# Kernel tuning notes

Measured on AMD Instinct MI355X. Metric: run time of the kernel, lower is better.

Reference implementation:

```python
import jax, jax.numpy as jnp
import numpy as np

N = 20000
E = 320000
F_IN = 50
HID = 64          # hidden_channels
HEADS = 8
WIDTH = HID * HEADS  # 512
NUM_CLASSES = 121


def setup_inputs() -> dict:
    key = jax.random.key(0)
    ks = jax.random.split(key, 16)
    def p(k, shape, fan_in):
        return (jax.random.normal(k, shape, dtype=jnp.float32) / np.sqrt(fan_in)).astype(jnp.float32)
    x = jax.random.normal(ks[0], (N, F_IN), dtype=jnp.float32)
    edge_index = jax.random.randint(ks[1], (2, E), 0, N, dtype=jnp.int64)
    return {
        "x": x,
        "edge_index": edge_index,
        # layer 1: 50 -> 64, heads=8, concat
        "W1": p(ks[2], (F_IN, HEADS * HID), F_IN),
        "a1_src": p(ks[3], (HEADS, HID), HID),
        "a1_dst": p(ks[4], (HEADS, HID), HID),
        "b1": jnp.zeros((HEADS * HID,), jnp.float32),
        # layer 2: 512 -> 512, heads=1, concat
        "W2": p(ks[5], (WIDTH, WIDTH), WIDTH),
        "a2_src": p(ks[6], (1, WIDTH), WIDTH),
        "a2_dst": p(ks[7], (1, WIDTH), WIDTH),
        "b2": jnp.zeros((WIDTH,), jnp.float32),
        # layer 3: 512 -> 121, heads=1, concat=False (mean)
        "W3": p(ks[8], (WIDTH, NUM_CLASSES), WIDTH),
        "a3_src": p(ks[9], (1, NUM_CLASSES), NUM_CLASSES),
        "a3_dst": p(ks[10], (1, NUM_CLASSES), NUM_CLASSES),
        "b3": jnp.zeros((NUM_CLASSES,), jnp.float32),
    }


def gat_conv(x, src, dst, W, a_src, a_dst, b, heads, out_ch, concat):
    n = x.shape[0]
    h = (x @ W).reshape(n, heads, out_ch)                 # [N, H, C]
    al_s = jnp.sum(h * a_src, axis=-1)                     # [N, H]
    al_d = jnp.sum(h * a_dst, axis=-1)                     # [N, H]
    e = jax.nn.leaky_relu(al_s[src] + al_d[dst], 0.2)      # [E, H]
    # edge softmax per destination node (stable)
    m = jax.ops.segment_max(e, dst, num_segments=n)        # [N, H]
    m = jnp.where(jnp.isfinite(m), m, 0.0)
    ex = jnp.exp(e - m[dst])
    z = jax.ops.segment_sum(ex, dst, num_segments=n)       # [N, H]
    alpha = ex / (z[dst] + 1e-16)                          # [E, H]
    msg = h[src] * alpha[..., None]                        # [E, H, C]
    out = jax.ops.segment_sum(msg, dst, num_segments=n)    # [N, H, C]
    out = out.reshape(n, heads * out_ch) if concat else out.mean(axis=1)
    return out + b


def reference(x, edge_index, W1, a1_src, a1_dst, b1, W2, a2_src, a2_dst, b2, W3, a3_src, a3_dst, b3):
    n = x.shape[0]
    # PyG GATConv adds self loops by default
    loops = jnp.arange(n, dtype=edge_index.dtype)
    src = jnp.concatenate([edge_index[0], loops])
    dst = jnp.concatenate([edge_index[1], loops])
    # eval mode: dropout is identity
    x1 = gat_conv(x, src, dst, W1, a1_src, a1_dst, b1, HEADS, HID, True)
    h = jax.nn.elu(x1)
    x1 = gat_conv(h, src, dst, W2, a2_src, a2_dst, b2, 1, WIDTH, True)
    h = jax.nn.elu(x1)
    x1 = gat_conv(h, src, dst, W3, a3_src, a3_dst, b3, 1, NUM_CLASSES, False)
    return x1
```

## Files before the change

kernel.cpp:

```cpp
#include <hip/hip_runtime.h>
#include <hip/hip_bf16.h>
#include <hip/hip_fp16.h>

#define NN     20000
#define ERAW   320000
#define ETOT   (ERAW + NN)
#define F_IN   50
#define HID    64
#define HEADS  8
#define WIDTH  512
#define NCLS   121
#define NCLS_P 128

typedef __attribute__((ext_vector_type(8))) __bf16 bf16x8;
typedef __attribute__((ext_vector_type(4))) float floatx4;

__device__ __forceinline__ unsigned short f32_to_bf16_rn(float f) {
  unsigned u = __float_as_uint(f);
  unsigned r = u + 0x7fffu + ((u >> 16) & 1u);
  return (unsigned short)(r >> 16);
}
__device__ __forceinline__ void split_one(float f, unsigned short& h,
                                          unsigned short& l) {
  h = f32_to_bf16_rn(f);
  float fh = __uint_as_float(((unsigned)h) << 16);
  l = f32_to_bf16_rn(f - fh);
}

__device__ __forceinline__ float2 u2f2(unsigned u) {
  __half2 hv = *reinterpret_cast<__half2*>(&u);
  return __half22float2(hv);
}

__device__ __forceinline__ void gll16(const unsigned short* g,
                                      const unsigned short* l) {
  __builtin_amdgcn_global_load_lds(
      (const __attribute__((address_space(1))) unsigned int*)(const void*)g,
      (__attribute__((address_space(3))) unsigned int*)(void*)l, 16, 0, 0);
}

#define PW_BLOCKS 449
__global__ __launch_bounds__(256) void prep_weights(
    const float* __restrict__ W1, const float* __restrict__ W2,
    const float* __restrict__ W3, const float* __restrict__ a1s,
    const float* __restrict__ a1d, unsigned short* __restrict__ w1hHi,
    unsigned short* __restrict__ w1hLo, unsigned short* __restrict__ w2tHi,
    unsigned short* __restrict__ w2tLo, unsigned short* __restrict__ w3tHi,
    unsigned short* __restrict__ w3tLo, float* __restrict__ w1as,
    float* __restrict__ w1ad) {
  __shared__ float t[32][33];
  const int b = blockIdx.x;
  if (b < 320) {
    const float* W;
    unsigned short *thi, *tlo;
    int M, Mp, bx, by;
    const int K = WIDTH;
    if (b < 256) {
      W = W2; thi = w2tHi; tlo = w2tLo; M = WIDTH; Mp = WIDTH;
      bx = b & 15; by = b >> 4;
    } else {
      int bb = b - 256;
      W = W3; thi = w3tHi; tlo = w3tLo; M = NCLS; Mp = NCLS_P;
      bx = bb & 15; by = bb >> 4;
    }
    int k0 = bx * 32, m0 = by * 32;
    int tx = threadIdx.x & 31, ty = threadIdx.x >> 5;
    #pragma unroll
    for (int r = 0; r < 4; ++r) {
      int k = k0 + ty + r * 8, m = m0 + tx;
      float v = 0.f;
      if (k < K && m < M) v = W[(size_t)k * M + m];
      t[ty + r * 8][tx] = v;
    }
    __syncthreads();
    #pragma unroll
    for (int r = 0; r < 4; ++r) {
      int m = m0 + ty + r * 8, k = k0 + tx;
      if (m < Mp && k < K) {
        unsigned short h, l;
        split_one(t[tx][ty + r * 8], h, l);
        thi[(size_t)m * K + k] = h;
        tlo[(size_t)m * K + k] = l;
      }
    }
  } else if (b < 448) {
    int idx = (b - 320) * 256 + threadIdx.x;
    if (idx < HEADS * HID * HID) {
      int hd = idx >> 12, rem = idx & 4095;
      int col = rem >> 6, k = rem & 63;
      float v = (k < F_IN) ? W1[(size_t)k * WIDTH + hd * HID + col] : 0.f;
      unsigned short h, l;
      split_one(v, h, l);
      w1hHi[idx] = h;
      w1hLo[idx] = l;
    }
  } else {
    for (int idx = threadIdx.x; idx < 2 * F_IN * HEADS; idx += 256) {
      int which = idx >= F_IN * HEADS;
      int r = which ? idx - F_IN * HEADS : idx;
      int k = r >> 3, h = r & 7;
      const float* a = which ? a1d : a1s;
      float s = 0.f;
      for (int c = 0; c < HID; ++c)
        s += W1[(size_t)k * WIDTH + h * HID + c] * a[h * HID + c];
      (which ? w1ad : w1as)[r] = s;
    }
  }
}

__global__ __launch_bounds__(256) void gemm_split_db(
    const unsigned short* __restrict__ Ahi, const unsigned short* __restrict__ Alo,
    const unsigned short* __restrict__ Bthi, const unsigned short* __restrict__ Btlo,
    __half* __restrict__ C16, int N, int K, int M, int Mp, int RB, int CB) {
  __shared__ unsigned short lds[32768];

  const int f = blockIdx.x;
  const int xcd = f & 7;
  const int g = f >> 3;
  const int cb = g % CB;
  const int rb = (g / CB) * 8 + xcd;
  if (rb >= RB) return;
  const int r0 = rb * 128, c0 = cb * 128;

  const int tid = threadIdx.x;
  const int wave = tid >> 6, lane = tid & 63;
  const int wr = wave >> 1, wc = wave & 1;
  const int lkg = lane >> 4, lmn = lane & 15;

  const int rquad = lane >> 2, slot = lane & 3;
  const unsigned short* abase =
      (wave == 0) ? Ahi : (wave == 1) ? Alo : (wave == 2) ? Bthi : Btlo;
  const bool isA = wave < 2;
  const unsigned short* gsrc[8];
  int ldsoff[8];
  #pragma unroll
  for (int i = 0; i < 8; ++i) {
    int r = i * 16 + rquad;
    int c = slot ^ ((r >> 1) & 3);
    size_t grow;
    if (isA) {
      int ra = r0 + r;
      if (ra > N - 1) ra = N - 1;
      grow = (size_t)ra;
    } else {
      grow = (size_t)(c0 + r);
    }
    gsrc[i] = abase + grow * K + c * 8;
    ldsoff[i] = wave * 4096 + i * 512;
  }

  int offA[4], offB[4];
  #pragma unroll
  for (int mi = 0; mi < 4; ++mi) {
    int m = wr * 64 + mi * 16 + lmn;
    offA[mi] = m * 32 + (lkg ^ ((m >> 1) & 3)) * 8;
  }
  #pragma unroll
  for (int ni = 0; ni < 4; ++ni) {
    int n = wc * 64 + ni * 16 + lmn;
    offB[ni] = 8192 + n * 32 + (lkg ^ ((n >> 1) & 3)) * 8;
  }

  floatx4 acc[4][4] = {};

  #pragma unroll
  for (int i = 0; i < 8; ++i) gll16(gsrc[i], lds + ldsoff[i]);

  const int nk = K >> 5;
  for (int t = 0; t < nk; ++t) {
    if (t + 1 < nk) {
      const unsigned short* dst = lds + ((t + 1) & 1) * 16384;
      #pragma unroll
      for (int i = 0; i < 8; ++i)
        gll16(gsrc[i] + (t + 1) * 32, dst + ldsoff[i]);
      asm volatile("s_waitcnt vmcnt(8)" ::: "memory");
    } else {
      asm volatile("s_waitcnt vmcnt(0)" ::: "memory");
    }
    __builtin_amdgcn_sched_barrier(0);
    __builtin_amdgcn_s_barrier();
    __builtin_amdgcn_sched_barrier(0);

    const unsigned short* Lb = lds + (t & 1) * 16384;
    bf16x8 fAhi[4], fAlo[4], fBhi[4], fBlo[4];
    #pragma unroll
    for (int mi = 0; mi < 4; ++mi) {
      fAhi[mi] = *(const bf16x8*)(Lb + offA[mi]);
      fAlo[mi] = *(const bf16x8*)(Lb + 4096 + offA[mi]);
    }
    #pragma unroll
    for (int ni = 0; ni < 4; ++ni) {
      fBhi[ni] = *(const bf16x8*)(Lb + offB[ni]);
      fBlo[ni] = *(const bf16x8*)(Lb + 4096 + offB[ni]);
    }
    #pragma unroll
    for (int mi = 0; mi < 4; ++mi)
      #pragma unroll
      for (int ni = 0; ni < 4; ++ni) {
        acc[mi][ni] = __builtin_amdgcn_mfma_f32_16x16x32_bf16(
            fAhi[mi], fBhi[ni], acc[mi][ni], 0, 0, 0);
        acc[mi][ni] = __builtin_amdgcn_mfma_f32_16x16x32_bf16(
            fAhi[mi], fBlo[ni], acc[mi][ni], 0, 0, 0);
        acc[mi][ni] = __builtin_amdgcn_mfma_f32_16x16x32_bf16(
            fAlo[mi], fBhi[ni], acc[mi][ni], 0, 0, 0);
      }

    __builtin_amdgcn_sched_barrier(0);
    asm volatile("s_waitcnt lgkmcnt(0)" ::: "memory");
    __builtin_amdgcn_s_barrier();
    __builtin_amdgcn_sched_barrier(0);
  }

  #pragma unroll
  for (int mi = 0; mi < 4; ++mi) {
    #pragma unroll
    for (int r = 0; r < 4; ++r) {
      int grow = r0 + wr * 64 + mi * 16 + (lane >> 4) * 4 + r;
      if (grow >= N) continue;
      #pragma unroll
      for (int ni = 0; ni < 4; ++ni) {
        int gcol = c0 + wc * 64 + ni * 16 + lmn;
        float v = (gcol < M) ? acc[mi][ni][r] : 0.f;
        C16[(size_t)grow * Mp + gcol] = __float2half(v);
      }
    }
  }
}

__global__ __launch_bounds__(256) void gemm_l1_heads(
    const unsigned short* __restrict__ Ahi, const unsigned short* __restrict__ Alo,
    const unsigned short* __restrict__ Bthi, const unsigned short* __restrict__ Btlo,
    unsigned short* __restrict__ outHi, unsigned short* __restrict__ outLo,
    const float* __restrict__ bias) {
  __shared__ unsigned short sAhi[8192], sAlo[8192], sBhi[4096], sBlo[4096];
  const int tid = threadIdx.x;
  const int wave = tid >> 6, lane = tid & 63;
  const int r0 = blockIdx.x * 128;
  const int hd = blockIdx.y;
  const int lkg = lane >> 4, lmn = lane & 15;

  #pragma unroll
  for (int t = 0; t < 4; ++t) {
    int cid = tid + t * 256;
    int row = cid >> 3, c = cid & 7;
    int gr = r0 + row; if (gr > NN - 1) gr = NN - 1;
    const size_t goff = (size_t)gr * WIDTH + hd * HID + c * 8;
    int loff = (((c >> 2) * 4 + (c & 3)) * 128 + row) * 8;
    *(uint4*)(sAhi + loff) = *(const uint4*)(Ahi + goff);
    *(uint4*)(sAlo + loff) = *(const uint4*)(Alo + goff);
  }
  #pragma unroll
  for (int t = 0; t < 2; ++t) {
    int cid = tid + t * 256;
    int col = cid >> 3, c = cid & 7;
    const size_t goff = (size_t)(hd * HID + col) * HID + c * 8;
    int loff = (((c >> 2) * 4 + (c & 3)) * 64 + col) * 8;
    *(uint4*)(sBhi + loff) = *(const uint4*)(Bthi + goff);
    *(uint4*)(sBlo + loff) = *(const uint4*)(Btlo + goff);
  }
  __syncthreads();

  floatx4 acc[2][4] = {};
  #pragma unroll
  for (int ks = 0; ks < 2; ++ks) {
    bf16x8 fAhi[2], fAlo[2], fBhi[4], fBlo[4];
    #pragma unroll
    for (int mi = 0; mi < 2; ++mi) {
      int m = wave * 32 + mi * 16 + lmn;
      int off = ((ks * 4 + lkg) * 128 + m) * 8;
      fAhi[mi] = *(const bf16x8*)(sAhi + off);
      fAlo[mi] = *(const bf16x8*)(sAlo + off);
    }
    #pragma unroll
    for (int ni = 0; ni < 4; ++ni) {
      int n = ni * 16 + lmn;
      int off = ((ks * 4 + lkg) * 64 + n) * 8;
      fBhi[ni] = *(const bf16x8*)(sBhi + off);
      fBlo[ni] = *(const bf16x8*)(sBlo + off);
    }
    #pragma unroll
    for (int mi = 0; mi < 2; ++mi)
      #pragma unroll
      for (int ni = 0; ni < 4; ++ni) {
        acc[mi][ni] = __builtin_amdgcn_mfma_f32_16x16x32_bf16(
            fAhi[mi], fBhi[ni], acc[mi][ni], 0, 0, 0);
        acc[mi][ni] = __builtin_amdgcn_mfma_f32_16x16x32_bf16(
            fAhi[mi], fBlo[ni], acc[mi][ni], 0, 0, 0);
        acc[mi][ni] = __builtin_amdgcn_mfma_f32_16x16x32_bf16(
            fAlo[mi], fBhi[ni], acc[mi][ni], 0, 0, 0);
      }
  }

  #pragma unroll
  for (int mi = 0; mi < 2; ++mi) {
    #pragma unroll
    for (int r = 0; r < 4; ++r) {
      int grow = r0 + wave * 32 + mi * 16 + (lane >> 4) * 4 + r;
      if (grow >= NN) continue;
      #pragma unroll
      for (int ni = 0; ni < 4; ++ni) {
        int gcol = hd * HID + ni * 16 + lmn;
        float v = acc[mi][ni][r] + bias[gcol];
        v = (v > 0.f) ? v : (__expf(v) - 1.0f);
        unsigned short hh, ll;
        split_one(v, hh, ll);
        outHi[(size_t)grow * WIDTH + gcol] = hh;
        outLo[(size_t)grow * WIDTH + gcol] = ll;
      }
    }
  }
}

__global__ __launch_bounds__(256) void al1_kernel(
    const float* __restrict__ x, const float* __restrict__ w1as,
    const float* __restrict__ w1ad, float* __restrict__ al_s,
    float* __restrict__ al_d) {
  int n = (blockIdx.x * blockDim.x + threadIdx.x) >> 6;
  int lane = threadIdx.x & 63;
  if (n >= NN) return;
  float xv = (lane < F_IN) ? x[(size_t)n * F_IN + lane] : 0.f;
  float ws[HEADS], wd[HEADS];
  #pragma unroll
  for (int h = 0; h < HEADS; ++h) {
    ws[h] = (lane < F_IN) ? w1as[lane * HEADS + h] : 0.f;
    wd[h] = (lane < F_IN) ? w1ad[lane * HEADS + h] : 0.f;
  }
  #pragma unroll
  for (int h = 0; h < HEADS; ++h) {
    float ss = xv * ws[h], sd = xv * wd[h];
    #pragma unroll
    for (int o = 32; o; o >>= 1) {
      ss += __shfl_xor(ss, o);
      sd += __shfl_xor(sd, o);
    }
    if (lane == 0) {
      al_s[n * HEADS + h] = ss;
      al_d[n * HEADS + h] = sd;
    }
  }
}

template <int C, int CS>
__global__ __launch_bounds__(256) void compute_al16(
    const __half* __restrict__ h16, const float* __restrict__ a_src,
    const float* __restrict__ a_dst, float* __restrict__ al_s,
    float* __restrict__ al_d) {
  int n = (blockIdx.x * blockDim.x + threadIdx.x) >> 6;
  int lane = threadIdx.x & 63;
  if (n >= NN) return;
  const __half* hr = h16 + (size_t)n * CS;
  float ss = 0.f, sd = 0.f;
  if (C % 512 == 0) {
    uint4 raw = *(const uint4*)(hr + lane * 8);
    float f[8];
    float2 t;
    t = u2f2(raw.x); f[0] = t.x; f[1] = t.y;
    t = u2f2(raw.y); f[2] = t.x; f[3] = t.y;
    t = u2f2(raw.z); f[4] = t.x; f[5] = t.y;
    t = u2f2(raw.w); f[6] = t.x; f[7] = t.y;
    #pragma unroll
    for (int j = 0; j < 8; ++j) {
      int c = lane * 8 + j;
      ss += f[j] * a_src[c];
      sd += f[j] * a_dst[c];
    }
  } else {
    for (int c = lane; c < C; c += 64) {
      float v = __half2float(hr[c]);
      ss += v * a_src[c];
      sd += v * a_dst[c];
    }
  }
  #pragma unroll
  for (int o = 32; o; o >>= 1) {
    ss += __shfl_xor(ss, o);
    sd += __shfl_xor(sd, o);
  }
  if (lane == 0) {
    al_s[n] = ss;
    al_d[n] = sd;
  }
}

__global__ __launch_bounds__(256) void count_deg(
    const int* __restrict__ edst, int* __restrict__ deg) {
  int e = blockIdx.x * blockDim.x + threadIdx.x;
  if (e >= ETOT) return;
  int d = (e < ERAW) ? edst[e] : (e - ERAW);
  atomicAdd(&deg[d], 1);
}

__global__ __launch_bounds__(256) void scan_deg(
    const int* __restrict__ deg, int* __restrict__ rowptr) {
  __shared__ int part[256];
  const int t = threadIdx.x;
  const int CHUNK = (NN + 255) / 256;
  int lo = t * CHUNK, hi = min(lo + CHUNK, NN);
  int s = 0;
  for (int i = lo; i < hi; ++i) s += deg[i];
  part[t] = s;
  __syncthreads();
  for (int off = 1; off < 256; off <<= 1) {
    int v = (t >= off) ? part[t - off] : 0;
    __syncthreads();
    part[t] += v;
    __syncthreads();
  }
  int base = (t == 0) ? 0 : part[t - 1];
  for (int i = lo; i < hi; ++i) {
    rowptr[i] = base;
    base += deg[i];
  }
  if (t == 255) rowptr[NN] = part[255];
}

__global__ __launch_bounds__(256) void scatter_csr(
    const int* __restrict__ esrc, const int* __restrict__ edst,
    const int* __restrict__ rowptr, int* __restrict__ cnt,
    int* __restrict__ csrc) {
  int e = blockIdx.x * blockDim.x + threadIdx.x;
  if (e >= ETOT) return;
  int s, d;
  if (e < ERAW) { s = esrc[e]; d = edst[e]; }
  else          { s = e - ERAW; d = e - ERAW; }
  int pos = rowptr[d] + atomicAdd(&cnt[d], 1);
  csrc[pos] = s;
}

__global__ __launch_bounds__(256) void agg_x_sm(
    const int* __restrict__ rowptr, const int* __restrict__ csrc,
    const float* __restrict__ al_s, const float* __restrict__ al_d,
    const float* __restrict__ x, unsigned short* __restrict__ outHi,
    unsigned short* __restrict__ outLo) {
  const int w = threadIdx.x >> 6, lane = threadIdx.x & 63;
  const int d = blockIdx.x * 4 + w;
  if (d >= NN) return;
  const int r0 = rowptr[d], r1 = rowptr[d + 1];
  const int mh = lane & 7;
  const float ald_my = al_d[d * HEADS + mh];
  float m_my = al_s[d * HEADS + mh] + ald_my;
  m_my = (m_my > 0.f) ? m_my : 0.2f * m_my;

  float z_my = 0.f;
  float acc[HEADS];
  #pragma unroll
  for (int hh = 0; hh < HEADS; ++hh) acc[hh] = 0.f;
  for (int p = r0; p < r1; ++p) {
    int s = csrc[p];
    float v = al_s[s * HEADS + mh] + ald_my;
    v = (v > 0.f) ? v : 0.2f * v;
    float a = __expf(v - m_my);
    z_my += a;
    float xv = (lane < F_IN) ? x[(size_t)s * F_IN + lane] : 0.f;
    #pragma unroll
    for (int hh = 0; hh < HEADS; ++hh) acc[hh] += __shfl(a, hh, 8) * xv;
  }
  #pragma unroll
  for (int hh = 0; hh < HEADS; ++hh) {
    float zh = __shfl(z_my, hh, 8);
    float v = (lane < F_IN) ? acc[hh] / (zh + 1e-16f) : 0.f;
    unsigned short h2, l2;
    split_one(v, h2, l2);
    outHi[(size_t)d * WIDTH + hh * HID + lane] = h2;
    outLo[(size_t)d * WIDTH + hh * HID + lane] = l2;
  }
}

template <int M, int MS, bool ELU, bool SPLIT>
__global__ __launch_bounds__(256) void pull_agg_sm(
    const int* __restrict__ rowptr, const int* __restrict__ csrc,
    const float* __restrict__ al_s, const float* __restrict__ al_d,
    const __half* __restrict__ h16, const float* __restrict__ bias,
    float* __restrict__ out, unsigned short* __restrict__ outHi,
    unsigned short* __restrict__ outLo) {
  constexpr int EPL = MS / 64;
  const int w = threadIdx.x >> 6;
  const int lane = threadIdx.x & 63;
  const int d = blockIdx.x * 4 + w;
  if (d >= NN) return;
  const int r0 = rowptr[d], r1 = rowptr[d + 1];
  const float ald = al_d[d];
  float m = al_s[d] + ald;
  m = (m > 0.f) ? m : 0.2f * m;

  const int base = lane * EPL;
  const __half* hb = h16 + base;
  float acc[EPL];
  #pragma unroll
  for (int j = 0; j < EPL; ++j) acc[j] = 0.f;
  float z = 0.f;

  int p = r0;
  for (; p + 8 <= r1; p += 8) {
    int s[8];
    #pragma unroll
    for (int j = 0; j < 8; ++j) s[j] = csrc[p + j];
    uint4 raw8[8];
    unsigned raw2[8];
    #pragma unroll
    for (int j = 0; j < 8; ++j) {
      const __half* hr = hb + (size_t)s[j] * MS;
      if (EPL == 8)      raw8[j] = *(const uint4*)hr;
      else if (EPL == 2) raw2[j] = *(const unsigned*)hr;
    }
    float av[8];
    #pragma unroll
    for (int j = 0; j < 8; ++j) av[j] = al_s[s[j]];
    #pragma unroll
    for (int j = 0; j < 8; ++j) {
      float v = av[j] + ald;
      v = (v > 0.f) ? v : 0.2f * v;
      float a = __expf(v - m);
      z += a;
      if (EPL == 8) {
        float2 f0 = u2f2(raw8[j].x), f1 = u2f2(raw8[j].y);
        float2 f2 = u2f2(raw8[j].z), f3 = u2f2(raw8[j].w);
        acc[0] += f0.x * a; acc[1] += f0.y * a;
        acc[2] += f1.x * a; acc[3] += f1.y * a;
        acc[4] += f2.x * a; acc[5] += f2.y * a;
        acc[6] += f3.x * a; acc[7] += f3.y * a;
      } else if (EPL == 2) {
        float2 f0 = u2f2(raw2[j]);
        acc[0] += f0.x * a;
        acc[1] += f0.y * a;
      }
    }
  }
  for (; p < r1; ++p) {
    int s = csrc[p];
    float v = al_s[s] + ald;
    v = (v > 0.f) ? v : 0.2f * v;
    float a = __expf(v - m);
    z += a;
    const __half* hr = hb + (size_t)s * MS;
    if (EPL == 8) {
      uint4 raw = *(const uint4*)hr;
      float2 f0 = u2f2(raw.x), f1 = u2f2(raw.y);
      float2 f2 = u2f2(raw.z), f3 = u2f2(raw.w);
      acc[0] += f0.x * a; acc[1] += f0.y * a;
      acc[2] += f1.x * a; acc[3] += f1.y * a;
      acc[4] += f2.x * a; acc[5] += f2.y * a;
      acc[6] += f3.x * a; acc[7] += f3.y * a;
    } else if (EPL == 2) {
      unsigned raw = *(const unsigned*)hr;
      float2 f0 = u2f2(raw);
      acc[0] += f0.x * a;
      acc[1] += f0.y * a;
    }
  }
  const float iz = 1.0f / (z + 1e-16f);

  #pragma unroll
  for (int j = 0; j < EPL; ++j) {
    if ((M == MS) || (base + j < M)) {
      float v = acc[j] * iz + bias[base + j];
      if (ELU) v = (v > 0.f) ? v : (__expf(v) - 1.0f);
      if (SPLIT) {
        unsigned short hh, ll;
        split_one(v, hh, ll);
        outHi[(size_t)d * M + base + j] = hh;
        outLo[(size_t)d * M + base + j] = ll;
      } else {
        out[(size_t)d * M + base + j] = v;
      }
    }
  }
}

extern "C" void kernel_launch(void* const* d_in, const int* in_sizes, int n_in,
                              void* d_out, int out_size, void* d_ws,
                              size_t ws_size, hipStream_t stream) {
  const float* x      = (const float*)d_in[0];
  const int*   ei     = (const int*)d_in[1];
  const float* W1     = (const float*)d_in[2];
  const float* a1_src = (const float*)d_in[3];
  const float* a1_dst = (const float*)d_in[4];
  const float* b1     = (const float*)d_in[5];
  const float* W2     = (const float*)d_in[6];
  const float* a2_src = (const float*)d_in[7];
  const float* a2_dst = (const float*)d_in[8];
  const float* b2     = (const float*)d_in[9];
  const float* W3     = (const float*)d_in[10];
  const float* a3_src = (const float*)d_in[11];
  const float* a3_dst = (const float*)d_in[12];
  const float* b3     = (const float*)d_in[13];
  float* out = (float*)d_out;

  const int* esrc = ei;
  const int* edst = ei + ERAW;

  unsigned short* p1Hi  = (unsigned short*)d_ws;
  unsigned short* p1Lo  = p1Hi + (size_t)NN * WIDTH;
  unsigned short* p2Hi  = p1Lo + (size_t)NN * WIDTH;
  unsigned short* p2Lo  = p2Hi + (size_t)NN * WIDTH;
  __half*        h16    = (__half*)(p2Lo + (size_t)NN * WIDTH);
  unsigned short* w1hHi = (unsigned short*)(h16 + (size_t)NN * WIDTH);
  unsigned short* w1hLo = w1hHi + (size_t)HEADS * HID * HID;
  unsigned short* w2tHi = w1hLo + (size_t)HEADS * HID * HID;
  unsigned short* w2tLo = w2tHi + (size_t)WIDTH * WIDTH;
  unsigned short* w3tHi = w2tLo + (size_t)WIDTH * WIDTH;
  unsigned short* w3tLo = w3tHi + (size_t)NCLS_P * WIDTH;
  float* al_s   = (float*)(w3tLo + (size_t)NCLS_P * WIDTH);
  float* al_d   = al_s + (size_t)NN * HEADS;
  float* w1as   = al_d + (size_t)NN * HEADS;
  float* w1ad   = w1as + F_IN * HEADS;
  int* deg      = (int*)(w1ad + F_IN * HEADS);
  int* cnt      = deg + NN;
  int* rowptr   = cnt + NN;
  int* csrc     = rowptr + NN + 4;

  hipMemsetAsync(deg, 0, (size_t)(2 * NN) * sizeof(int), stream);
  const int eblk = (ETOT + 255) / 256;
  count_deg<<<eblk, 256, 0, stream>>>(edst, deg);
  scan_deg<<<1, 256, 0, stream>>>(deg, rowptr);
  scatter_csr<<<eblk, 256, 0, stream>>>(esrc, edst, rowptr, cnt, csrc);

  prep_weights<<<PW_BLOCKS, 256, 0, stream>>>(
      W1, W2, W3, a1_src, a1_dst, w1hHi, w1hLo, w2tHi, w2tLo, w3tHi, w3tLo,
      w1as, w1ad);

  const int nwblk = (NN + 3) / 4;

  al1_kernel<<<nwblk, 256, 0, stream>>>(x, w1as, w1ad, al_s, al_d);
  agg_x_sm<<<nwblk, 256, 0, stream>>>(rowptr, csrc, al_s, al_d, x, p1Hi,
                                      p1Lo);
  gemm_l1_heads<<<dim3((NN + 127) / 128, HEADS), 256, 0, stream>>>(
      p1Hi, p1Lo, w1hHi, w1hLo, p2Hi, p2Lo, b1);

  const int RB = (NN + 127) / 128;
  const int RBG = (RB + 7) / 8;

  gemm_split_db<<<RBG * 8 * (WIDTH / 128), 256, 0, stream>>>(
      p2Hi, p2Lo, w2tHi, w2tLo, h16, NN, WIDTH, WIDTH, WIDTH, RB, WIDTH / 128);
  compute_al16<WIDTH, WIDTH><<<nwblk, 256, 0, stream>>>(h16, a2_src, a2_dst,
                                                        al_s, al_d);
  pull_agg_sm<WIDTH, WIDTH, true, true><<<nwblk, 256, 0, stream>>>(
      rowptr, csrc, al_s, al_d, h16, b2, nullptr, p1Hi, p1Lo);

  gemm_split_db<<<RBG * 8 * (NCLS_P / 128), 256, 0, stream>>>(
      p1Hi, p1Lo, w3tHi, w3tLo, h16, NN, WIDTH, NCLS, NCLS_P, RB,
      NCLS_P / 128);
  compute_al16<NCLS, NCLS_P><<<nwblk, 256, 0, stream>>>(h16, a3_src, a3_dst,
                                                        al_s, al_d);
  pull_agg_sm<NCLS, NCLS_P, false, false><<<nwblk, 256, 0, stream>>>(
      rowptr, csrc, al_s, al_d, h16, b3, out, nullptr, nullptr);
}
```

Measured before the change: 398.9 us.

## Double GEMM K-tile to 64 with 8-way swizzle and batch edge loads in agg_x

The split-bf16 GEMM now stages a K-slice of 64 instead of 32 per iteration. It doubles LDS to 128 KB, switches to an 8-slot XOR swizzle, and runs two MFMA sub-steps per barrier pair, so barrier and wait overhead per unit of work is halved. The layer-1 aggregation kernel unrolls the edge loop by 8 and issues all neighbour index, feature and attention loads before computing, to expose more memory-level parallelism. The larger LDS footprint cuts blocks per CU and may hurt occupancy and latency hiding.

```diff
diff --git a/kernel.cpp b/kernel.cpp
--- a/kernel.cpp
+++ b/kernel.cpp
@@ -112,7 +112,7 @@
     const unsigned short* __restrict__ Ahi, const unsigned short* __restrict__ Alo,
     const unsigned short* __restrict__ Bthi, const unsigned short* __restrict__ Btlo,
     __half* __restrict__ C16, int N, int K, int M, int Mp, int RB, int CB) {
-  __shared__ unsigned short lds[32768];
+  __shared__ unsigned short lds[65536];
 
   const int f = blockIdx.x;
   const int xcd = f & 7;
@@ -127,16 +127,16 @@
   const int wr = wave >> 1, wc = wave & 1;
   const int lkg = lane >> 4, lmn = lane & 15;
 
-  const int rquad = lane >> 2, slot = lane & 3;
+  const int row8 = lane >> 3, cslot = lane & 7;
   const unsigned short* abase =
       (wave == 0) ? Ahi : (wave == 1) ? Alo : (wave == 2) ? Bthi : Btlo;
   const bool isA = wave < 2;
-  const unsigned short* gsrc[8];
-  int ldsoff[8];
-  #pragma unroll
-  for (int i = 0; i < 8; ++i) {
-    int r = i * 16 + rquad;
-    int c = slot ^ ((r >> 1) & 3);
+  const unsigned short* gsrc[16];
+  int ldsoff[16];
+  #pragma unroll
+  for (int i = 0; i < 16; ++i) {
+    int r = i * 8 + row8;
+    int c = cslot ^ (r & 7);
     size_t grow;
     if (isA) {
       int ra = r0 + r;
@@ -146,34 +146,34 @@
       grow = (size_t)(c0 + r);
     }
     gsrc[i] = abase + grow * K + c * 8;
-    ldsoff[i] = wave * 4096 + i * 512;
-  }
-
-  int offA[4], offB[4];
+    ldsoff[i] = wave * 8192 + i * 512;
+  }
+
+  int rowA[4], m7A[4], rowB[4], m7B[4];
   #pragma unroll
   for (int mi = 0; mi < 4; ++mi) {
     int m = wr * 64 + mi * 16 + lmn;
-    offA[mi] = m * 32 + (lkg ^ ((m >> 1) & 3)) * 8;
+    rowA[mi] = m * 64;  m7A[mi] = m & 7;
   }
   #pragma unroll
   for (int ni = 0; ni < 4; ++ni) {
     int n = wc * 64 + ni * 16 + lmn;
-    offB[ni] = 8192 + n * 32 + (lkg ^ ((n >> 1) & 3)) * 8;
+    rowB[ni] = 16384 + n * 64;  m7B[ni] = n & 7;
   }
 
   floatx4 acc[4][4] = {};
 
   #pragma unroll
-  for (int i = 0; i < 8; ++i) gll16(gsrc[i], lds + ldsoff[i]);
-
-  const int nk = K >> 5;
+  for (int i = 0; i < 16; ++i) gll16(gsrc[i], lds + ldsoff[i]);
+
+  const int nk = K >> 6;
   for (int t = 0; t < nk; ++t) {
     if (t + 1 < nk) {
-      const unsigned short* dst = lds + ((t + 1) & 1) * 16384;
-      #pragma unroll
-      for (int i = 0; i < 8; ++i)
-        gll16(gsrc[i] + (t + 1) * 32, dst + ldsoff[i]);
-      asm volatile("s_waitcnt vmcnt(8)" ::: "memory");
+      const unsigned short* dst = lds + ((t + 1) & 1) * 32768;
+      #pragma unroll
+      for (int i = 0; i < 16; ++i)
+        gll16(gsrc[i] + (t + 1) * 64, dst + ldsoff[i]);
+      asm volatile("s_waitcnt vmcnt(16)" ::: "memory");
     } else {
       asm volatile("s_waitcnt vmcnt(0)" ::: "memory");
     }
@@ -181,29 +181,34 @@
     __builtin_amdgcn_s_barrier();
     __builtin_amdgcn_sched_barrier(0);
 
-    const unsigned short* Lb = lds + (t & 1) * 16384;
-    bf16x8 fAhi[4], fAlo[4], fBhi[4], fBlo[4];
-    #pragma unroll
-    for (int mi = 0; mi < 4; ++mi) {
-      fAhi[mi] = *(const bf16x8*)(Lb + offA[mi]);
-      fAlo[mi] = *(const bf16x8*)(Lb + 4096 + offA[mi]);
-    }
-    #pragma unroll
-    for (int ni = 0; ni < 4; ++ni) {
-      fBhi[ni] = *(const bf16x8*)(Lb + offB[ni]);
-      fBlo[ni] = *(const bf16x8*)(Lb + 4096 + offB[ni]);
-    }
-    #pragma unroll
-    for (int mi = 0; mi < 4; ++mi)
+    const unsigned short* Lb = lds + (t & 1) * 32768;
+    #pragma unroll
+    for (int ksub = 0; ksub < 2; ++ksub) {
+      bf16x8 fAhi[4], fAlo[4], fBhi[4], fBlo[4];
+      #pragma unroll
+      for (int mi = 0; mi < 4; ++mi) {
+        int s = rowA[mi] + (((ksub << 2) | lkg) ^ m7A[mi]) * 8;
+        fAhi[mi] = *(const bf16x8*)(Lb + s);
+        fAlo[mi] = *(const bf16x8*)(Lb + s + 8192);
+      }
       #pragma unroll
       for (int ni = 0; ni < 4; ++ni) {
-        acc[mi][ni] = __builtin_amdgcn_mfma_f32_16x16x32_bf16(
-            fAhi[mi], fBhi[ni], acc[mi][ni], 0, 0, 0);
-        acc[mi][ni] = __builtin_amdgcn_mfma_f32_16x16x32_bf16(
-            fAhi[mi], fBlo[ni], acc[mi][ni], 0, 0, 0);
-        acc[mi][ni] = __builtin_amdgcn_mfma_f32_16x16x32_bf16(
-            fAlo[mi], fBhi[ni], acc[mi][ni], 0, 0, 0);
-      }
+        int s = rowB[ni] + (((ksub << 2) | lkg) ^ m7B[ni]) * 8;
+        fBhi[ni] = *(const bf16x8*)(Lb + s);
+        fBlo[ni] = *(const bf16x8*)(Lb + s + 8192);
+      }
+      #pragma unroll
+      for (int mi = 0; mi < 4; ++mi)
+        #pragma unroll
+        for (int ni = 0; ni < 4; ++ni) {
+          acc[mi][ni] = __builtin_amdgcn_mfma_f32_16x16x32_bf16(
+              fAhi[mi], fBhi[ni], acc[mi][ni], 0, 0, 0);
+          acc[mi][ni] = __builtin_amdgcn_mfma_f32_16x16x32_bf16(
+              fAhi[mi], fBlo[ni], acc[mi][ni], 0, 0, 0);
+          acc[mi][ni] = __builtin_amdgcn_mfma_f32_16x16x32_bf16(
+              fAlo[mi], fBhi[ni], acc[mi][ni], 0, 0, 0);
+        }
+    }
 
     __builtin_amdgcn_sched_barrier(0);
     asm volatile("s_waitcnt lgkmcnt(0)" ::: "memory");
@@ -445,7 +450,30 @@
   float acc[HEADS];
   #pragma unroll
   for (int hh = 0; hh < HEADS; ++hh) acc[hh] = 0.f;
-  for (int p = r0; p < r1; ++p) {
+
+  int p = r0;
+  for (; p + 8 <= r1; p += 8) {
+    int s[8];
+    #pragma unroll
+    for (int j = 0; j < 8; ++j) s[j] = csrc[p + j];
+    float xv[8];
+    #pragma unroll
+    for (int j = 0; j < 8; ++j)
+      xv[j] = (lane < F_IN) ? x[(size_t)s[j] * F_IN + lane] : 0.f;
+    float av[8];
+    #pragma unroll
+    for (int j = 0; j < 8; ++j) av[j] = al_s[s[j] * HEADS + mh];
+    #pragma unroll
+    for (int j = 0; j < 8; ++j) {
+      float v = av[j] + ald_my;
+      v = (v > 0.f) ? v : 0.2f * v;
+      float a = __expf(v - m_my);
+      z_my += a;
+      #pragma unroll
+      for (int hh = 0; hh < HEADS; ++hh) acc[hh] += __shfl(a, hh, 8) * xv[j];
+    }
+  }
+  for (; p < r1; ++p) {
     int s = csrc[p];
     float v = al_s[s * HEADS + mh] + ald_my;
     v = (v > 0.f) ? v : 0.2f * v;
@@ -455,6 +483,7 @@
     #pragma unroll
     for (int hh = 0; hh < HEADS; ++hh) acc[hh] += __shfl(a, hh, 8) * xv;
   }
+
   #pragma unroll
   for (int hh = 0; hh < HEADS; ++hh) {
     float zh = __shfl(z_my, hh, 8);
```

Result: no change. 400.8 us (+0.5%).
